# Kernel tuning notes

Hardware: AMD Instinct MI355X
Metric: run time of the kernel (lower is better)

Reference implementation:

```python
import jax, jax.numpy as jnp
import numpy as np


def setup_inputs() -> dict:
    key = jax.random.key(0)
    k1, k2, k3 = jax.random.split(key, 3)
    B, K, IN, OUT = 4096, 8, 1024, 1024
    x = jax.random.normal(k1, (B, IN), dtype=jnp.float32)
    blend_weights = jax.random.uniform(k2, (B, K), dtype=jnp.float32)
    weight = jax.random.normal(k3, (K, OUT, IN), dtype=jnp.float32) * 0.01
    bias = jnp.zeros((K, OUT), dtype=jnp.float32)
    return {"x": x, "blend_weights": blend_weights, "weight": weight, "bias": bias}


def reference(x, blend_weights, weight, bias):
    # Mathematically identical to blending weights first then matvec:
    #   einsum('bk,koi->boi') then bmm  ==  per-expert GEMM then blend.
    # per-expert outputs: (b, k, o)
    expert_out = jnp.einsum('bi,koi->bko', x, weight)
    out = jnp.einsum('bk,bko->bo', blend_weights, expert_out)
    out = out + blend_weights @ bias  # (b,k) @ (k,o) -> (b,o)
    return out
```

## Files before the change

### kernel.cpp

```cpp
#include <hip/hip_runtime.h>
#include <hip/hip_bf16.h>
#include <stdint.h>

typedef short short8 __attribute__((ext_vector_type(8)));
typedef float f32x4  __attribute__((ext_vector_type(4)));
typedef unsigned short u16;

#define B_ROWS 4096
#define NEXP   8
#define IN_D   1024
#define OUT_D  1024

#define BM 128
#define BN 128
#define BK 64

__device__ __forceinline__ u16 f2bf(float f) {
    uint32_t u = __float_as_uint(f);
    uint32_t r = (u + 0x7fffu + ((u >> 16) & 1u)) >> 16;
    return (u16)r;
}

__global__ __launch_bounds__(256) void build_a(const float* __restrict__ x,
                                               const float* __restrict__ bwt,
                                               u16* __restrict__ a) {
    const int t = blockIdx.x * 256 + threadIdx.x;
    const int b = t >> 8, i4 = t & 255;
    float4 v = reinterpret_cast<const float4*>(x)[(size_t)b * 256 + i4];
    float4 w0 = reinterpret_cast<const float4*>(bwt)[b * 2];
    float4 w1 = reinterpret_cast<const float4*>(bwt)[b * 2 + 1];
    float wk[8] = {w0.x, w0.y, w0.z, w0.w, w1.x, w1.y, w1.z, w1.w};
    #pragma unroll
    for (int k = 0; k < NEXP; ++k) {
        ushort4 o;
        o.x = f2bf(wk[k] * v.x); o.y = f2bf(wk[k] * v.y);
        o.z = f2bf(wk[k] * v.z); o.w = f2bf(wk[k] * v.w);
        reinterpret_cast<ushort4*>(a)[((size_t)k * B_ROWS + b) * 256 + i4] = o;
    }
}

__global__ __launch_bounds__(256) void cvt_bf16(const float* __restrict__ in,
                                                u16* __restrict__ out, int n4) {
    int i = blockIdx.x * 256 + threadIdx.x;
    if (i >= n4) return;
    float4 v = reinterpret_cast<const float4*>(in)[i];
    ushort4 o;
    o.x = f2bf(v.x); o.y = f2bf(v.y); o.z = f2bf(v.z); o.w = f2bf(v.w);
    reinterpret_cast<ushort4*>(out)[i] = o;
}

__device__ __forceinline__ void glds16(const u16* g, u16* lds_base, int off_bytes) {
    auto gp = (const __attribute__((address_space(1))) void*)(uintptr_t)(g);
    auto lp = (__attribute__((address_space(3))) void*)(uintptr_t)((const char*)lds_base + off_bytes);
    __builtin_amdgcn_global_load_lds(gp, lp, 16, 0, 0);
}

__global__ __launch_bounds__(256) void moe_gemm(
    const u16* __restrict__ Ab,
    const u16* __restrict__ Wb,
    float* __restrict__ out0,
    float* __restrict__ out1,
    int epb)
{
    __shared__ __align__(16) u16 As[BM * BK];
    __shared__ __align__(16) u16 Bs[BN * BK];

    const int tid  = threadIdx.x;
    const int lane = tid & 63, wid = tid >> 6;
    const int wm = wid >> 1, wn = wid & 1;
    const int lr = lane & 15, lg = lane >> 4;
    const int bn = blockIdx.x * BN;
    const int bm = blockIdx.y * BM;
    const int bz = blockIdx.z;

    int st_row[4], st_col[4], st_off[4];
    #pragma unroll
    for (int r = 0; r < 4; ++r) {
        int c = r * 256 + wid * 64 + lane;
        st_row[r] = c >> 3;
        st_col[r] = (c & 7) * 8;
        st_off[r] = (r * 256 + wid * 64) * 16;
    }

    f32x4 acc[4][4];
    #pragma unroll
    for (int mi = 0; mi < 4; ++mi)
        #pragma unroll
        for (int ni = 0; ni < 4; ++ni)
            acc[mi][ni] = (f32x4){0.f, 0.f, 0.f, 0.f};

    const int nsteps = IN_D / BK;
    for (int e = 0; e < epb; ++e) {
        const int kexp = bz * epb + e;
        const u16* Ak = Ab + (size_t)kexp * B_ROWS * IN_D;
        const u16* Wk = Wb + (size_t)kexp * OUT_D * IN_D;

        for (int it = 0; it < nsteps; ++it) {
            const int i0 = it * BK;
            __syncthreads();
            #pragma unroll
            for (int r = 0; r < 4; ++r) {
                glds16(Ak + (size_t)(bm + st_row[r]) * IN_D + i0 + st_col[r], As, st_off[r]);
                glds16(Wk + (size_t)(bn + st_row[r]) * IN_D + i0 + st_col[r], Bs, st_off[r]);
            }
            __syncthreads();

            #pragma unroll
            for (int ks = 0; ks < 2; ++ks) {
                short8 a[4], b[4];
                #pragma unroll
                for (int mi = 0; mi < 4; ++mi)
                    a[mi] = *(const short8*)(As + (wm * 64 + mi * 16 + lr) * BK + ks * 32 + lg * 8);
                #pragma unroll
                for (int ni = 0; ni < 4; ++ni)
                    b[ni] = *(const short8*)(Bs + (wn * 64 + ni * 16 + lr) * BK + ks * 32 + lg * 8);
                #pragma unroll
                for (int mi = 0; mi < 4; ++mi)
                    #pragma unroll
                    for (int ni = 0; ni < 4; ++ni)
                        acc[mi][ni] = __builtin_amdgcn_mfma_f32_16x16x32_bf16(
                            a[mi], b[ni], acc[mi][ni], 0, 0, 0);
            }
        }
    }

    float* op = (bz == 0) ? out0 : out1;
    #pragma unroll
    for (int mi = 0; mi < 4; ++mi)
        #pragma unroll
        for (int ni = 0; ni < 4; ++ni)
            #pragma unroll
            for (int r = 0; r < 4; ++r) {
                const int grow = bm + wm * 64 + mi * 16 + lg * 4 + r;
                const int gcol = bn + wn * 64 + ni * 16 + lr;
                op[(size_t)grow * OUT_D + gcol] = acc[mi][ni][r];
            }
}

__global__ __launch_bounds__(256) void reduce_bias(
    const float* __restrict__ parts, const float* __restrict__ bwt,
    const float* __restrict__ bias, float* __restrict__ out, int np)
{
    const int i4 = blockIdx.x * 256 + threadIdx.x;
    const size_t total = (size_t)B_ROWS * OUT_D;
    const size_t base = (size_t)i4 * 4;
    if (base >= total) return;
    const int brow = (int)(base >> 10);
    const int o = (int)(base & 1023);

    float4 s = *reinterpret_cast<const float4*>(out + base);
    for (int z = 0; z < np; ++z) {
        float4 p = *reinterpret_cast<const float4*>(parts + (size_t)z * total + base);
        s.x += p.x; s.y += p.y; s.z += p.z; s.w += p.w;
    }
    #pragma unroll
    for (int k = 0; k < NEXP; ++k) {
        const float w = bwt[brow * NEXP + k];
        float4 bb = *reinterpret_cast<const float4*>(bias + k * OUT_D + o);
        s.x += w * bb.x; s.y += w * bb.y; s.z += w * bb.z; s.w += w * bb.w;
    }
    *reinterpret_cast<float4*>(out + base) = s;
}

__global__ __launch_bounds__(256) void naive_moe(
    const float* __restrict__ x, const float* __restrict__ bwt,
    const float* __restrict__ wgt, const float* __restrict__ bias,
    float* __restrict__ out)
{
    __shared__ float xs[IN_D];
    const int brow = blockIdx.x;
    const int o = blockIdx.y * 256 + threadIdx.x;
    for (int i = threadIdx.x; i < IN_D; i += 256) xs[i] = x[(size_t)brow * IN_D + i];
    __syncthreads();
    float acc = 0.f;
    for (int k = 0; k < NEXP; ++k) {
        const float* wr = wgt + ((size_t)k * OUT_D + o) * IN_D;
        float d = 0.f;
        for (int i = 0; i < IN_D; ++i) d += xs[i] * wr[i];
        acc += bwt[brow * NEXP + k] * (d + bias[k * OUT_D + o]);
    }
    out[(size_t)brow * OUT_D + o] = acc;
}

extern "C" void kernel_launch(void* const* d_in, const int* in_sizes, int n_in,
                              void* d_out, int out_size, void* d_ws, size_t ws_size,
                              hipStream_t stream) {
    const float* x    = (const float*)d_in[0];
    const float* bwt  = (const float*)d_in[1];
    const float* wgt  = (const float*)d_in[2];
    const float* bias = (const float*)d_in[3];
    float* out = (float*)d_out;

    const size_t a_bytes    = (size_t)NEXP * B_ROWS * IN_D * 2;
    const size_t w_bytes    = (size_t)NEXP * OUT_D * IN_D * 2;
    const size_t part_bytes = (size_t)B_ROWS * OUT_D * 4;

    if (ws_size < a_bytes + w_bytes) {
        naive_moe<<<dim3(B_ROWS, OUT_D / 256), 256, 0, stream>>>(x, bwt, wgt, bias, out);
        return;
    }

    u16* ab = (u16*)d_ws;
    u16* wb = (u16*)((char*)d_ws + a_bytes);
    float* parts = (float*)((char*)d_ws + a_bytes + w_bytes);

    const int nz = (ws_size >= a_bytes + w_bytes + part_bytes) ? 2 : 1;

    build_a<<<B_ROWS, 256, 0, stream>>>(x, bwt, ab);
    cvt_bf16<<<(NEXP * OUT_D * IN_D / 4 + 255) / 256, 256, 0, stream>>>(
        wgt, wb, NEXP * OUT_D * IN_D / 4);

    if (nz == 2) {
        moe_gemm<<<dim3(OUT_D / BN, B_ROWS / BM, 2), 256, 0, stream>>>(ab, wb, parts, out, NEXP / 2);
        reduce_bias<<<((B_ROWS * OUT_D / 4) + 255) / 256, 256, 0, stream>>>(parts, bwt, bias, out, 1);
    } else {
        moe_gemm<<<dim3(OUT_D / BN, B_ROWS / BM, 1), 256, 0, stream>>>(ab, wb, out, out, NEXP);
        reduce_bias<<<((B_ROWS * OUT_D / 4) + 255) / 256, 256, 0, stream>>>(nullptr, bwt, bias, out, 0);
    }
}
```

Measured before the change: 205.7 us.

## Fuse prep kernels, add XCD-aware tile swizzle and four-way expert split

Merges the bf16 weight conversion and the blended-activation build into one launch. The GEMM switches to a 1D grid with a swizzle that groups consecutive tiles onto the same XCD, improving L2 reuse of A and W. When the workspace allows, it splits experts four ways instead of two, doubling the workgroup count. The cost is extra partial buffers that the reduce kernel must read.

```diff
diff --git a/kernel.cpp b/kernel.cpp
--- a/kernel.cpp
+++ b/kernel.cpp
@@ -21,32 +21,34 @@
     return (u16)r;
 }
 
-__global__ __launch_bounds__(256) void build_a(const float* __restrict__ x,
-                                               const float* __restrict__ bwt,
-                                               u16* __restrict__ a) {
-    const int t = blockIdx.x * 256 + threadIdx.x;
-    const int b = t >> 8, i4 = t & 255;
-    float4 v = reinterpret_cast<const float4*>(x)[(size_t)b * 256 + i4];
-    float4 w0 = reinterpret_cast<const float4*>(bwt)[b * 2];
-    float4 w1 = reinterpret_cast<const float4*>(bwt)[b * 2 + 1];
-    float wk[8] = {w0.x, w0.y, w0.z, w0.w, w1.x, w1.y, w1.z, w1.w};
-    #pragma unroll
-    for (int k = 0; k < NEXP; ++k) {
+#define W_CVT_BLOCKS 8192
+__global__ __launch_bounds__(256) void prep(const float* __restrict__ x,
+                                            const float* __restrict__ bwt,
+                                            const float* __restrict__ wgt,
+                                            u16* __restrict__ ab,
+                                            u16* __restrict__ wb) {
+    const int bid = blockIdx.x;
+    if (bid < W_CVT_BLOCKS) {
+        const int i = bid * 256 + threadIdx.x;
+        float4 v = reinterpret_cast<const float4*>(wgt)[i];
         ushort4 o;
-        o.x = f2bf(wk[k] * v.x); o.y = f2bf(wk[k] * v.y);
-        o.z = f2bf(wk[k] * v.z); o.w = f2bf(wk[k] * v.w);
-        reinterpret_cast<ushort4*>(a)[((size_t)k * B_ROWS + b) * 256 + i4] = o;
-    }
-}
-
-__global__ __launch_bounds__(256) void cvt_bf16(const float* __restrict__ in,
-                                                u16* __restrict__ out, int n4) {
-    int i = blockIdx.x * 256 + threadIdx.x;
-    if (i >= n4) return;
-    float4 v = reinterpret_cast<const float4*>(in)[i];
-    ushort4 o;
-    o.x = f2bf(v.x); o.y = f2bf(v.y); o.z = f2bf(v.z); o.w = f2bf(v.w);
-    reinterpret_cast<ushort4*>(out)[i] = o;
+        o.x = f2bf(v.x); o.y = f2bf(v.y); o.z = f2bf(v.z); o.w = f2bf(v.w);
+        reinterpret_cast<ushort4*>(wb)[i] = o;
+    } else {
+        const int b = bid - W_CVT_BLOCKS;
+        const int i4 = threadIdx.x;
+        float4 v = reinterpret_cast<const float4*>(x)[(size_t)b * 256 + i4];
+        float4 w0 = reinterpret_cast<const float4*>(bwt)[b * 2];
+        float4 w1 = reinterpret_cast<const float4*>(bwt)[b * 2 + 1];
+        float wk[8] = {w0.x, w0.y, w0.z, w0.w, w1.x, w1.y, w1.z, w1.w};
+        #pragma unroll
+        for (int k = 0; k < NEXP; ++k) {
+            ushort4 o;
+            o.x = f2bf(wk[k] * v.x); o.y = f2bf(wk[k] * v.y);
+            o.z = f2bf(wk[k] * v.z); o.w = f2bf(wk[k] * v.w);
+            reinterpret_cast<ushort4*>(ab)[((size_t)k * B_ROWS + b) * 256 + i4] = o;
+        }
+    }
 }
 
 __device__ __forceinline__ void glds16(const u16* g, u16* lds_base, int off_bytes) {
@@ -58,20 +60,26 @@
 __global__ __launch_bounds__(256) void moe_gemm(
     const u16* __restrict__ Ab,
     const u16* __restrict__ Wb,
-    float* __restrict__ out0,
-    float* __restrict__ out1,
-    int epb)
+    float* __restrict__ parts,
+    float* __restrict__ out,
+    int epb, int nz)
 {
     __shared__ __align__(16) u16 As[BM * BK];
     __shared__ __align__(16) u16 Bs[BN * BK];
+
+    const int nwg = gridDim.x;
+    const int cpx = nwg >> 3;
+    const int id  = blockIdx.x;
+    const int swz = (id & 7) * cpx + (id >> 3);
+    const int bz  = swz >> 8;
+    const int rem = swz & 255;
+    const int bm  = (rem >> 3) * BM;
+    const int bn  = (rem & 7) * BN;
 
     const int tid  = threadIdx.x;
     const int lane = tid & 63, wid = tid >> 6;
     const int wm = wid >> 1, wn = wid & 1;
     const int lr = lane & 15, lg = lane >> 4;
-    const int bn = blockIdx.x * BN;
-    const int bm = blockIdx.y * BM;
-    const int bz = blockIdx.z;
 
     int st_row[4], st_col[4], st_off[4];
     #pragma unroll
@@ -124,7 +132,7 @@
         }
     }
 
-    float* op = (bz == 0) ? out0 : out1;
+    float* op = (bz == nz - 1) ? out : parts + (size_t)bz * B_ROWS * OUT_D;
     #pragma unroll
     for (int mi = 0; mi < 4; ++mi)
         #pragma unroll
@@ -200,21 +208,18 @@
         return;
     }
 
+    int nz = 1;
+    if      (ws_size >= a_bytes + w_bytes + 3 * part_bytes) nz = 4;
+    else if (ws_size >= a_bytes + w_bytes + 1 * part_bytes) nz = 2;
+
     u16* ab = (u16*)d_ws;
     u16* wb = (u16*)((char*)d_ws + a_bytes);
     float* parts = (float*)((char*)d_ws + a_bytes + w_bytes);
 
-    const int nz = (ws_size >= a_bytes + w_bytes + part_bytes) ? 2 : 1;
-
-    build_a<<<B_ROWS, 256, 0, stream>>>(x, bwt, ab);
-    cvt_bf16<<<(NEXP * OUT_D * IN_D / 4 + 255) / 256, 256, 0, stream>>>(
-        wgt, wb, NEXP * OUT_D * IN_D / 4);
-
-    if (nz == 2) {
-        moe_gemm<<<dim3(OUT_D / BN, B_ROWS / BM, 2), 256, 0, stream>>>(ab, wb, parts, out, NEXP / 2);
-        reduce_bias<<<((B_ROWS * OUT_D / 4) + 255) / 256, 256, 0, stream>>>(parts, bwt, bias, out, 1);
-    } else {
-        moe_gemm<<<dim3(OUT_D / BN, B_ROWS / BM, 1), 256, 0, stream>>>(ab, wb, out, out, NEXP);
-        reduce_bias<<<((B_ROWS * OUT_D / 4) + 255) / 256, 256, 0, stream>>>(nullptr, bwt, bias, out, 0);
-    }
-}
+    prep<<<W_CVT_BLOCKS + B_ROWS, 256, 0, stream>>>(x, bwt, wgt, ab, wb);
+
+    moe_gemm<<<256 * nz, 256, 0, stream>>>(ab, wb, parts, out, NEXP / nz, nz);
+
+    reduce_bias<<<(B_ROWS * OUT_D / 4 + 255) / 256, 256, 0, stream>>>(
+        parts, bwt, bias, out, nz - 1);
+}
```

Result: slower. 211.6 us (+2.8%).
